# Performance work log

Hardware: AMD Instinct MI355X
Metric: run time of the kernel (lower is better)

The kernel has to match this reference:

```python
import jax, jax.numpy as jnp
import numpy as np

A_BITS = 8
W_BITS = 8
STRIDE = 1
PADDING = 1


def _quant_dequant(t, bits):
    """Symmetric per-tensor min-max quantize-dequantize to `bits` bits.

    This is the math the PCILT lookup-table conv realizes: every LUT entry is
    (quantized activation level) * (quantized weight level), so summing LUT
    entries over the conv window == conv(x_qdq, w_qdq).
    """
    qmax = 2.0 ** (bits - 1) - 1.0
    scale = jnp.maximum(jnp.max(jnp.abs(t)) / qmax, 1e-8)
    return jnp.clip(jnp.round(t / scale), -qmax, qmax) * scale


def setup_inputs() -> dict:
    key = jax.random.key(0)
    k1, k2 = jax.random.split(key)
    x = jax.random.normal(k1, (16, 64, 112, 112), dtype=jnp.float32)  # NCHW
    W = jax.random.normal(k2, (128, 64, 3, 3), dtype=jnp.float32) * 0.05  # OIHW
    return {"x": x, "W": W}


def reference(x, W):
    xq = _quant_dequant(x, A_BITS)
    wq = _quant_dequant(W, W_BITS)
    out = jax.lax.conv_general_dilated(
        xq, wq,
        window_strides=(STRIDE, STRIDE),
        padding=[(PADDING, PADDING), (PADDING, PADDING)],
        dimension_numbers=("NCHW", "OIHW", "NCHW"))
    return out  # [16, 128, 112, 112]
```

## Files before the change

### kernel.cpp

```cpp
#include <hip/hip_runtime.h>
#include <hip/hip_bf16.h>


typedef __attribute__((ext_vector_type(8))) short short8;
typedef __attribute__((ext_vector_type(4))) float f32x4;
typedef __attribute__((ext_vector_type(4))) float float4v;

#define N_IMG 16
#define C_IN 64
#define HW 112
#define O_CH 128
#define K_TOT 576
#define TPITCH 72
#define NPART 3136

__global__ __launch_bounds__(256) void absmax_part(const float* __restrict__ x,
                                                   const float* __restrict__ w,
                                                   float* __restrict__ part) {
    const int b = blockIdx.x, tid = threadIdx.x;
    const float4v* x4 = (const float4v*)x;
    const long base = (long)b * 1024 + tid;
    const float4v v0 = x4[base];
    const float4v v1 = x4[base + 256];
    const float4v v2 = x4[base + 512];
    const float4v v3 = x4[base + 768];
    float mx = fmaxf(fmaxf(fmaxf(fabsf(v0.x), fabsf(v0.y)), fmaxf(fabsf(v0.z), fabsf(v0.w))),
                     fmaxf(fmaxf(fabsf(v1.x), fabsf(v1.y)), fmaxf(fabsf(v1.z), fabsf(v1.w))));
    mx = fmaxf(mx, fmaxf(fmaxf(fabsf(v2.x), fabsf(v2.y)), fmaxf(fabsf(v2.z), fabsf(v2.w))));
    mx = fmaxf(mx, fmaxf(fmaxf(fabsf(v3.x), fabsf(v3.y)), fmaxf(fabsf(v3.z), fabsf(v3.w))));
    float mw = 0.f;
    if (b < 72) {
        const float4v q = ((const float4v*)w)[b * 256 + tid];
        mw = fmaxf(fmaxf(fabsf(q.x), fabsf(q.y)), fmaxf(fabsf(q.z), fabsf(q.w)));
    }
    #pragma unroll
    for (int off = 32; off > 0; off >>= 1) {
        mx = fmaxf(mx, __shfl_down(mx, off));
        mw = fmaxf(mw, __shfl_down(mw, off));
    }
    __shared__ float smx[4], smw[4];
    const int wave = tid >> 6, lane = tid & 63;
    if (lane == 0) { smx[wave] = mx; smw[wave] = mw; }
    __syncthreads();
    if (tid == 0) {
        part[b]         = fmaxf(fmaxf(smx[0], smx[1]), fmaxf(smx[2], smx[3]));
        part[NPART + b] = fmaxf(fmaxf(smw[0], smw[1]), fmaxf(smw[2], smw[3]));
    }
}

__global__ __launch_bounds__(256) void reduce_scal(const float* __restrict__ part,
                                                   unsigned* __restrict__ scal) {
    const int tid = threadIdx.x;
    float mx = 0.f, mw = 0.f;
    for (int i = tid; i < NPART; i += 256) {
        mx = fmaxf(mx, part[i]);
        mw = fmaxf(mw, part[NPART + i]);
    }
    #pragma unroll
    for (int off = 32; off > 0; off >>= 1) {
        mx = fmaxf(mx, __shfl_down(mx, off));
        mw = fmaxf(mw, __shfl_down(mw, off));
    }
    __shared__ float smx[4], smw[4];
    const int wave = tid >> 6, lane = tid & 63;
    if (lane == 0) { smx[wave] = mx; smw[wave] = mw; }
    __syncthreads();
    if (tid == 0) {
        scal[0] = __float_as_uint(fmaxf(fmaxf(smx[0], smx[1]), fmaxf(smx[2], smx[3])));
        scal[1] = __float_as_uint(fmaxf(fmaxf(smw[0], smw[1]), fmaxf(smw[2], smw[3])));
    }
}

__global__ __launch_bounds__(256) void quant_w(const float* __restrict__ w,
                                               const unsigned* __restrict__ scal,
                                               __hip_bfloat16* __restrict__ wt) {
    const int idx = blockIdx.x * 256 + threadIdx.x;
    if (idx >= O_CH * C_IN * 9) return;
    const float sw = fmaxf(__uint_as_float(scal[1]) * (1.f / 127.f), 1e-8f);
    const int kw = idx % 3;
    int t = idx / 3;
    const int kh = t % 3;
    t /= 3;
    const int c = t % C_IN;
    const int o = t / C_IN;
    float v = rintf(w[idx] / sw);
    v = fminf(fmaxf(v, -127.f), 127.f);
    wt[o * K_TOT + (kh * 3 + kw) * C_IN + c] = __float2bfloat16(v);
}

__global__ __launch_bounds__(256) void quant_x(const float* __restrict__ x,
                                               const unsigned* __restrict__ scal,
                                               unsigned short* __restrict__ xq) {
    __shared__ __align__(16) unsigned short tile[HW * TPITCH];
    const int tid = threadIdx.x;
    const int n = blockIdx.x / HW, h = blockIdx.x % HW;
    const float inv_sx = 1.f / fmaxf(__uint_as_float(scal[0]) * (1.f / 127.f), 1e-8f);
    #pragma unroll
    for (int i = 0; i < 7; ++i) {
        const int l = i * 256 + tid;
        const int c = l / 28, w4 = l - c * 28;
        const float4v v = *(const float4v*)(x + ((long)(n * C_IN + c) * HW + h) * HW + w4 * 4);
        float q[4];
        q[0] = fminf(fmaxf(rintf(v.x * inv_sx), -127.f), 127.f);
        q[1] = fminf(fmaxf(rintf(v.y * inv_sx), -127.f), 127.f);
        q[2] = fminf(fmaxf(rintf(v.z * inv_sx), -127.f), 127.f);
        q[3] = fminf(fmaxf(rintf(v.w * inv_sx), -127.f), 127.f);
        const int osw = ((c >> 3) ^ (w4 & 7)) * 8 + (c & 7);
        #pragma unroll
        for (int j = 0; j < 4; ++j) {
            const __hip_bfloat16 b = __float2bfloat16(q[j]);
            tile[(w4 * 4 + j) * TPITCH + osw] = *(const unsigned short*)&b;
        }
    }
    __syncthreads();
    const int cw = tid & 7, wi = tid >> 3;
    unsigned short* dst = xq + ((long)(n * HW + h) * HW) * C_IN;
    #pragma unroll
    for (int j = 0; j < 4; ++j) {
        const int w = j * 32 + wi;
        if (w < HW) {
            const int osrc = (cw ^ ((w >> 2) & 7)) * 8;
            *(short8*)(dst + w * C_IN + cw * 8) = *(const short8*)(tile + w * TPITCH + osrc);
        }
    }
}

__global__ __launch_bounds__(256) void conv_kernel(const unsigned short* __restrict__ xq,
                                                   const unsigned short* __restrict__ wtp,
                                                   const unsigned* __restrict__ scal,
                                                   float* __restrict__ out) {
    __shared__ __align__(16) unsigned short xs[3 * 114 * TPITCH];
    const int tid = threadIdx.x;
    const int wave = tid >> 6, lane = tid & 63;
    const int quad = lane >> 4, l16 = lane & 15;
    const int lin = (blockIdx.x & 7) * 224 + (blockIdx.x >> 3);
    const int n = lin / HW, oh = lin % HW;

    if (tid < 48) {
        const int r = tid >> 4, col = (tid >> 3) & 1, c8 = tid & 7;
        *(short8*)(xs + (r * 114 + col * 113) * TPITCH + c8 * 8) = (short8)0;
    }
    #pragma unroll
    for (int it = 0; it < 11; ++it) {
        const int g = it * 256 + tid;
        if (g < 2688) {
            const int r = g / 896, rem = g - r * 896;
            const int ow = rem >> 3, c8 = rem & 7;
            const int ih = oh - 1 + r;
            short8 v = (short8)0;
            if ((unsigned)ih < (unsigned)HW)
                v = *(const short8*)(xq + (((long)(n * HW + ih) * HW + ow) * C_IN) + c8 * 8);
            *(short8*)(xs + (r * 114 + ow + 1) * TPITCH + c8 * 8) = v;
        }
    }

    f32x4 acc[7][2];
    #pragma unroll
    for (int mt = 0; mt < 7; ++mt) { acc[mt][0] = (f32x4)0.f; acc[mt][1] = (f32x4)0.f; }

    const unsigned short* wrow0 = wtp + (wave * 32 + l16) * K_TOT + quad * 8;
    const unsigned short* wrow1 = wrow0 + 16 * K_TOT;

    short8 bcur[2][2], bnxt[2][2];
    #pragma unroll
    for (int half = 0; half < 2; ++half) {
        bcur[half][0] = *(const short8*)(wrow0 + half * 32);
        bcur[half][1] = *(const short8*)(wrow1 + half * 32);
    }

    __syncthreads();

    #pragma unroll
    for (int tap = 0; tap < 9; ++tap) {
        if (tap < 8) {
            #pragma unroll
            for (int half = 0; half < 2; ++half) {
                bnxt[half][0] = *(const short8*)(wrow0 + (tap + 1) * C_IN + half * 32);
                bnxt[half][1] = *(const short8*)(wrow1 + (tap + 1) * C_IN + half * 32);
            }
        }
        const unsigned short* rowb = xs + (tap / 3) * (114 * TPITCH) + (tap % 3) * TPITCH + l16 * TPITCH + quad * 8;
        #pragma unroll
        for (int half = 0; half < 2; ++half) {
            #pragma unroll
            for (int mt = 0; mt < 7; ++mt) {
                const short8 afr = *(const short8*)(rowb + mt * (16 * TPITCH) + half * 32);
                acc[mt][0] = __builtin_amdgcn_mfma_f32_16x16x32_bf16(afr, bcur[half][0], acc[mt][0], 0, 0, 0);
                acc[mt][1] = __builtin_amdgcn_mfma_f32_16x16x32_bf16(afr, bcur[half][1], acc[mt][1], 0, 0, 0);
            }
        }
        #pragma unroll
        for (int half = 0; half < 2; ++half) {
            bcur[half][0] = bnxt[half][0];
            bcur[half][1] = bnxt[half][1];
        }
    }

    const float s = fmaxf(__uint_as_float(scal[0]) * (1.f / 127.f), 1e-8f) *
                    fmaxf(__uint_as_float(scal[1]) * (1.f / 127.f), 1e-8f);
    #pragma unroll
    for (int mt = 0; mt < 7; ++mt) {
        #pragma unroll
        for (int ot = 0; ot < 2; ++ot) {
            const int o = wave * 32 + ot * 16 + l16;
            const int mrow = mt * 16 + quad * 4;
            const f32x4 v = acc[mt][ot] * s;
            *(f32x4*)(out + (((long)(n * O_CH + o) * HW + oh) * HW + mrow)) = v;
        }
    }
}

extern "C" void kernel_launch(void* const* d_in, const int* in_sizes, int n_in,
                              void* d_out, int out_size, void* d_ws, size_t ws_size,
                              hipStream_t stream) {
    const float* x = (const float*)d_in[0];
    const float* W = (const float*)d_in[1];
    float* out = (float*)d_out;

    unsigned* scal = (unsigned*)d_ws;
    __hip_bfloat16* wt = (__hip_bfloat16*)((char*)d_ws + 1024);
    unsigned short* xq = (unsigned short*)((char*)d_ws + 148480);
    float* part = (float*)xq;

    hipLaunchKernelGGL(absmax_part, dim3(NPART), dim3(256), 0, stream, x, W, part);
    hipLaunchKernelGGL(reduce_scal, dim3(1), dim3(256), 0, stream, part, scal);
    hipLaunchKernelGGL(quant_w, dim3(288), dim3(256), 0, stream, W, scal, wt);
    hipLaunchKernelGGL(quant_x, dim3(N_IMG * HW), dim3(256), 0, stream, x, scal, xq);
    hipLaunchKernelGGL(conv_kernel, dim3(N_IMG * HW), dim3(256), 0, stream, xq, (const unsigned short*)wt, scal, out);
}
```

Baseline: 198.8 us.

## Switch quantized conv from bf16 MFMA to int8 MFMA with int32 accumulation

Quantized activations and weights are now stored as int8 instead of bf16 integer values, and the conv uses the i32_16x16x64_i8 MFMA with int32 accumulators converted to float at the end. This halves the memory traffic for the quantized intermediate and the shared-memory tile, and halves the MFMA instruction count per tap. The shared tile pitch changes to 80 bytes, and launch bounds now request 4 blocks per CU. Integer accumulation is exact, so results should match the reference up to the final scale multiply.

```diff
diff --git a/kernel.cpp b/kernel.cpp
--- a/kernel.cpp
+++ b/kernel.cpp
@@ -3,15 +3,19 @@
 
 
 typedef __attribute__((ext_vector_type(8))) short short8;
+typedef __attribute__((ext_vector_type(4))) int   int4v;
 typedef __attribute__((ext_vector_type(4))) float f32x4;
 typedef __attribute__((ext_vector_type(4))) float float4v;
+typedef __attribute__((ext_vector_type(8)))  signed char char8;
+typedef __attribute__((ext_vector_type(16))) signed char char16;
 
 #define N_IMG 16
 #define C_IN 64
 #define HW 112
 #define O_CH 128
-#define K_TOT 576
-#define TPITCH 72
+#define WPITCH 576
+#define XPITCH 80
+#define TP 72
 #define NPART 3136
 
 __global__ __launch_bounds__(256) void absmax_part(const float* __restrict__ x,
@@ -73,7 +77,7 @@
 
 __global__ __launch_bounds__(256) void quant_w(const float* __restrict__ w,
                                                const unsigned* __restrict__ scal,
-                                               __hip_bfloat16* __restrict__ wt) {
+                                               signed char* __restrict__ wt8) {
     const int idx = blockIdx.x * 256 + threadIdx.x;
     if (idx >= O_CH * C_IN * 9) return;
     const float sw = fmaxf(__uint_as_float(scal[1]) * (1.f / 127.f), 1e-8f);
@@ -85,13 +89,13 @@
     const int o = t / C_IN;
     float v = rintf(w[idx] / sw);
     v = fminf(fmaxf(v, -127.f), 127.f);
-    wt[o * K_TOT + (kh * 3 + kw) * C_IN + c] = __float2bfloat16(v);
+    wt8[o * WPITCH + (kh * 3 + kw) * C_IN + c] = (signed char)(int)v;
 }
 
 __global__ __launch_bounds__(256) void quant_x(const float* __restrict__ x,
                                                const unsigned* __restrict__ scal,
-                                               unsigned short* __restrict__ xq) {
-    __shared__ __align__(16) unsigned short tile[HW * TPITCH];
+                                               signed char* __restrict__ xq8) {
+    __shared__ __align__(16) short tile[HW * TP];
     const int tid = threadIdx.x;
     const int n = blockIdx.x / HW, h = blockIdx.x % HW;
     const float inv_sx = 1.f / fmaxf(__uint_as_float(scal[0]) * (1.f / 127.f), 1e-8f);
@@ -107,93 +111,85 @@
         q[3] = fminf(fmaxf(rintf(v.w * inv_sx), -127.f), 127.f);
         const int osw = ((c >> 3) ^ (w4 & 7)) * 8 + (c & 7);
         #pragma unroll
-        for (int j = 0; j < 4; ++j) {
-            const __hip_bfloat16 b = __float2bfloat16(q[j]);
-            tile[(w4 * 4 + j) * TPITCH + osw] = *(const unsigned short*)&b;
-        }
-    }
-    __syncthreads();
-    const int cw = tid & 7, wi = tid >> 3;
-    unsigned short* dst = xq + ((long)(n * HW + h) * HW) * C_IN;
-    #pragma unroll
-    for (int j = 0; j < 4; ++j) {
-        const int w = j * 32 + wi;
+        for (int j = 0; j < 4; ++j)
+            tile[(w4 * 4 + j) * TP + osw] = (short)q[j];
+    }
+    __syncthreads();
+    const int g = tid & 3, wi = tid >> 2;
+    signed char* dst = xq8 + (long)(n * HW + h) * HW * C_IN;
+    #pragma unroll
+    for (int j = 0; j < 2; ++j) {
+        const int w = j * 64 + wi;
         if (w < HW) {
-            const int osrc = (cw ^ ((w >> 2) & 7)) * 8;
-            *(short8*)(dst + w * C_IN + cw * 8) = *(const short8*)(tile + w * TPITCH + osrc);
-        }
-    }
-}
-
-__global__ __launch_bounds__(256) void conv_kernel(const unsigned short* __restrict__ xq,
-                                                   const unsigned short* __restrict__ wtp,
-                                                   const unsigned* __restrict__ scal,
-                                                   float* __restrict__ out) {
-    __shared__ __align__(16) unsigned short xs[3 * 114 * TPITCH];
+            const int sw = (w >> 2) & 7;
+            const short8 s0 = *(const short8*)(tile + w * TP + ((2 * g) ^ sw) * 8);
+            const short8 s1 = *(const short8*)(tile + w * TP + ((2 * g + 1) ^ sw) * 8);
+            const char8 c0 = __builtin_convertvector(s0, char8);
+            const char8 c1 = __builtin_convertvector(s1, char8);
+            const char16 cc = __builtin_shufflevector(c0, c1,
+                0, 1, 2, 3, 4, 5, 6, 7, 8, 9, 10, 11, 12, 13, 14, 15);
+            *(char16*)(dst + w * C_IN + g * 16) = cc;
+        }
+    }
+}
+
+__global__ __launch_bounds__(256, 4) void conv_kernel(const signed char* __restrict__ xq8,
+                                                      const signed char* __restrict__ wt8,
+                                                      const unsigned* __restrict__ scal,
+                                                      float* __restrict__ out) {
+    __shared__ __align__(16) signed char xs[3 * 114 * XPITCH];
     const int tid = threadIdx.x;
     const int wave = tid >> 6, lane = tid & 63;
     const int quad = lane >> 4, l16 = lane & 15;
     const int lin = (blockIdx.x & 7) * 224 + (blockIdx.x >> 3);
     const int n = lin / HW, oh = lin % HW;
 
-    if (tid < 48) {
-        const int r = tid >> 4, col = (tid >> 3) & 1, c8 = tid & 7;
-        *(short8*)(xs + (r * 114 + col * 113) * TPITCH + c8 * 8) = (short8)0;
-    }
-    #pragma unroll
-    for (int it = 0; it < 11; ++it) {
-        const int g = it * 256 + tid;
-        if (g < 2688) {
-            const int r = g / 896, rem = g - r * 896;
-            const int ow = rem >> 3, c8 = rem & 7;
+    if (tid < 24) {
+        const int r = tid >> 3, col = (tid >> 2) & 1, c16 = tid & 3;
+        *(int4v*)(xs + (r * 114 + col * 113) * XPITCH + c16 * 16) = (int4v)0;
+    }
+    #pragma unroll
+    for (int it = 0; it < 6; ++it) {
+        const int gph = it * 256 + tid;
+        if (gph < 1344) {
+            const int r = gph / 448, rem = gph - r * 448;
+            const int ow = rem >> 2, c16 = rem & 3;
             const int ih = oh - 1 + r;
-            short8 v = (short8)0;
+            int4v v = (int4v)0;
             if ((unsigned)ih < (unsigned)HW)
-                v = *(const short8*)(xq + (((long)(n * HW + ih) * HW + ow) * C_IN) + c8 * 8);
-            *(short8*)(xs + (r * 114 + ow + 1) * TPITCH + c8 * 8) = v;
-        }
-    }
-
-    f32x4 acc[7][2];
-    #pragma unroll
-    for (int mt = 0; mt < 7; ++mt) { acc[mt][0] = (f32x4)0.f; acc[mt][1] = (f32x4)0.f; }
-
-    const unsigned short* wrow0 = wtp + (wave * 32 + l16) * K_TOT + quad * 8;
-    const unsigned short* wrow1 = wrow0 + 16 * K_TOT;
-
-    short8 bcur[2][2], bnxt[2][2];
-    #pragma unroll
-    for (int half = 0; half < 2; ++half) {
-        bcur[half][0] = *(const short8*)(wrow0 + half * 32);
-        bcur[half][1] = *(const short8*)(wrow1 + half * 32);
-    }
+                v = *(const int4v*)(xq8 + ((long)(n * HW + ih) * HW + ow) * C_IN + c16 * 16);
+            *(int4v*)(xs + (r * 114 + ow + 1) * XPITCH + c16 * 16) = v;
+        }
+    }
+
+    int4v acc[7][2];
+    #pragma unroll
+    for (int mt = 0; mt < 7; ++mt) { acc[mt][0] = (int4v)0; acc[mt][1] = (int4v)0; }
+
+    const signed char* wrow0 = wt8 + (wave * 32 + l16) * WPITCH + quad * 16;
+    const signed char* wrow1 = wrow0 + 16 * WPITCH;
+
+    int4v bcur0 = *(const int4v*)(wrow0);
+    int4v bcur1 = *(const int4v*)(wrow1);
+    int4v bnxt0, bnxt1;
 
     __syncthreads();
 
     #pragma unroll
     for (int tap = 0; tap < 9; ++tap) {
         if (tap < 8) {
-            #pragma unroll
-            for (int half = 0; half < 2; ++half) {
-                bnxt[half][0] = *(const short8*)(wrow0 + (tap + 1) * C_IN + half * 32);
-                bnxt[half][1] = *(const short8*)(wrow1 + (tap + 1) * C_IN + half * 32);
-            }
-        }
-        const unsigned short* rowb = xs + (tap / 3) * (114 * TPITCH) + (tap % 3) * TPITCH + l16 * TPITCH + quad * 8;
+            bnxt0 = *(const int4v*)(wrow0 + (tap + 1) * C_IN);
+            bnxt1 = *(const int4v*)(wrow1 + (tap + 1) * C_IN);
+        }
+        const signed char* rowb = xs + ((tap / 3) * 114 + (tap % 3) + l16) * XPITCH + quad * 16;
         #pragma unroll
-        for (int half = 0; half < 2; ++half) {
-            #pragma unroll
-            for (int mt = 0; mt < 7; ++mt) {
-                const short8 afr = *(const short8*)(rowb + mt * (16 * TPITCH) + half * 32);
-                acc[mt][0] = __builtin_amdgcn_mfma_f32_16x16x32_bf16(afr, bcur[half][0], acc[mt][0], 0, 0, 0);
-                acc[mt][1] = __builtin_amdgcn_mfma_f32_16x16x32_bf16(afr, bcur[half][1], acc[mt][1], 0, 0, 0);
-            }
-        }
-        #pragma unroll
-        for (int half = 0; half < 2; ++half) {
-            bcur[half][0] = bnxt[half][0];
-            bcur[half][1] = bnxt[half][1];
-        }
+        for (int mt = 0; mt < 7; ++mt) {
+            const int4v afr = *(const int4v*)(rowb + mt * (16 * XPITCH));
+            acc[mt][0] = __builtin_amdgcn_mfma_i32_16x16x64_i8(afr, bcur0, acc[mt][0], 0, 0, 0);
+            acc[mt][1] = __builtin_amdgcn_mfma_i32_16x16x64_i8(afr, bcur1, acc[mt][1], 0, 0, 0);
+        }
+        bcur0 = bnxt0;
+        bcur1 = bnxt1;
     }
 
     const float s = fmaxf(__uint_as_float(scal[0]) * (1.f / 127.f), 1e-8f) *
@@ -204,7 +200,7 @@
         for (int ot = 0; ot < 2; ++ot) {
             const int o = wave * 32 + ot * 16 + l16;
             const int mrow = mt * 16 + quad * 4;
-            const f32x4 v = acc[mt][ot] * s;
+            const f32x4 v = __builtin_convertvector(acc[mt][ot], f32x4) * s;
             *(f32x4*)(out + (((long)(n * O_CH + o) * HW + oh) * HW + mrow)) = v;
         }
     }
@@ -218,13 +214,13 @@
     float* out = (float*)d_out;
 
     unsigned* scal = (unsigned*)d_ws;
-    __hip_bfloat16* wt = (__hip_bfloat16*)((char*)d_ws + 1024);
-    unsigned short* xq = (unsigned short*)((char*)d_ws + 148480);
-    float* part = (float*)xq;
+    signed char* wt8 = (signed char*)((char*)d_ws + 1024);
+    signed char* xq8 = (signed char*)((char*)d_ws + 76800);
+    float* part = (float*)xq8;
 
     hipLaunchKernelGGL(absmax_part, dim3(NPART), dim3(256), 0, stream, x, W, part);
     hipLaunchKernelGGL(reduce_scal, dim3(1), dim3(256), 0, stream, part, scal);
-    hipLaunchKernelGGL(quant_w, dim3(288), dim3(256), 0, stream, W, scal, wt);
-    hipLaunchKernelGGL(quant_x, dim3(N_IMG * HW), dim3(256), 0, stream, x, scal, xq);
-    hipLaunchKernelGGL(conv_kernel, dim3(N_IMG * HW), dim3(256), 0, stream, xq, (const unsigned short*)wt, scal, out);
-}
+    hipLaunchKernelGGL(quant_w, dim3(288), dim3(256), 0, stream, W, scal, wt8);
+    hipLaunchKernelGGL(quant_x, dim3(N_IMG * HW), dim3(256), 0, stream, x, scal, xq8);
+    hipLaunchKernelGGL(conv_kernel, dim3(N_IMG * HW), dim3(256), 0, stream, xq8, wt8, scal, out);
+}
```

Measured after the change: 171.4 us. 13.8% less time.
